# Performance work log

Measured on AMD Instinct MI355X. Metric: run time of the kernel, lower is better.

The kernel has to match this reference:

```python
import jax, jax.numpy as jnp
import numpy as np

NUM_BLOCKS = 6
NUM_HEADS = 8
DIM = 49
SCALE = float(np.sqrt(DIM) + 1e-6)  # sqrt(49)+eps as in the torch code


def setup_inputs() -> dict:
    key = jax.random.key(0)
    ks = jax.random.split(key, 16)
    B, P = 64, 512
    s = 0.1  # keep activations well-scaled
    return {
        "embedding": jax.random.normal(ks[0], (B, P, DIM), jnp.float32),
        "target_labels": jax.random.randint(ks[1], (B,), 0, 10),
        "Wq": jax.random.normal(ks[2], (NUM_BLOCKS, NUM_HEADS, DIM, DIM), jnp.float32) * s,
        "bq": jax.random.normal(ks[3], (NUM_BLOCKS, NUM_HEADS, DIM), jnp.float32) * s,
        "Wk": jax.random.normal(ks[4], (NUM_BLOCKS, NUM_HEADS, DIM, DIM), jnp.float32) * s,
        "bk": jax.random.normal(ks[5], (NUM_BLOCKS, NUM_HEADS, DIM), jnp.float32) * s,
        "Wv": jax.random.normal(ks[6], (NUM_BLOCKS, NUM_HEADS, DIM, DIM), jnp.float32) * s,
        "bv": jax.random.normal(ks[7], (NUM_BLOCKS, NUM_HEADS, DIM), jnp.float32) * s,
        "Wh": jax.random.normal(ks[8], (NUM_BLOCKS, NUM_HEADS, DIM, DIM), jnp.float32) * s,
        "bh": jax.random.normal(ks[9], (NUM_BLOCKS, NUM_HEADS, DIM), jnp.float32) * s,
        "Wout": jax.random.normal(ks[10], (NUM_BLOCKS, DIM, NUM_HEADS * DIM), jnp.float32) * s,
        "W1": jax.random.normal(ks[11], (25, DIM), jnp.float32) * s,
        "b1": jax.random.normal(ks[12], (25,), jnp.float32) * s,
        "W2": jax.random.normal(ks[13], (10, 25), jnp.float32) * s,
        "b2": jax.random.normal(ks[14], (10,), jnp.float32) * s,
    }


def reference(embedding, target_labels, Wq, bq, Wk, bk, Wv, bv, Wh, bh, Wout, W1, b1, W2, b2):
    B, P, D = embedding.shape
    x = embedding
    for l in range(NUM_BLOCKS):  # fixed small structural loop over blocks
        # per-head projections, all heads batched: [B,H,P,D]
        Q = jnp.einsum('bpi,hoi->bhpo', x, Wq[l]) + bq[l][:, None, :]
        K = jnp.einsum('bpi,hoi->bhpo', x, Wk[l]) + bk[l][:, None, :]
        V = jnp.einsum('bpi,hoi->bhpo', x, Wv[l]) + bv[l][:, None, :]
        scores = jnp.einsum('bhpo,bhqo->bhpq', Q, K) / SCALE
        scores = jnp.clip(scores, -30.0, 30.0)
        weights = jax.nn.softmax(scores, axis=-1)
        attn_out = jnp.einsum('bhpq,bhqo->bhpo', weights, V)
        head_out = jnp.einsum('bhpo,hdo->bhpd', attn_out, Wh[l]) + bh[l][:, None, :]
        # concat head outputs along feature dim (head order preserved): [B,P,H*D]
        concat = head_out.transpose(0, 2, 1, 3).reshape(B, P, NUM_HEADS * D)
        # out-projection uses weight only (no bias), as in the torch forward
        x = jnp.einsum('bpc,oc->bpo', concat, Wout[l])
    pooled = x.mean(axis=1)  # [B, D]
    h = jax.nn.relu(pooled @ W1.T + b1)
    logits = h @ W2.T + b2  # [B, 10]
    logp = jax.nn.log_softmax(logits, axis=-1)
    loss = -jnp.take_along_axis(logp, target_labels[:, None], axis=1).mean()
    return loss
```

## Files before the change

kernel.cpp:

```cpp
#include <hip/hip_runtime.h>
#include <hip/hip_bf16.h>
#include <math.h>

#define Bn 64
#define Pn 512
#define Hn 8
#define Ln 6

typedef __bf16 bf16x8 __attribute__((ext_vector_type(8)));
typedef float f32x4 __attribute__((ext_vector_type(4)));

#define VMCNT(n) asm volatile("s_waitcnt vmcnt(" #n ")" ::: "memory")
#define LGKM0()  asm volatile("s_waitcnt lgkmcnt(0)" ::: "memory")

static __device__ __forceinline__ unsigned short f2bf(float f) {
    return __builtin_bit_cast(unsigned short, __float2bfloat16(f));
}
static __device__ __forceinline__ float bf2f(unsigned short v) {
    unsigned int u = ((unsigned int)v) << 16;
    return __builtin_bit_cast(float, u);
}
static __device__ __forceinline__ float fexp2(float x) {
    float r;
    asm("v_exp_f32 %0, %1" : "=v"(r) : "v"(x));
    return r;
}
static __device__ __forceinline__ unsigned cvtpk(float a, float b) {
    unsigned r;
    asm("v_cvt_pk_bf16_f32 %0, %1, %2" : "=v"(r) : "v"(a), "v"(b));
    return r;
}

#define C1F (1.4426950408889634f / 7.000001f)
#define C2F 43.2808512f

__global__ __launch_bounds__(256)
void prep_wqkv_kernel(const float* __restrict__ Wq, const float* __restrict__ Wk,
                      const float* __restrict__ Wv, unsigned short* __restrict__ out) {
    int idx = blockIdx.x * 256 + threadIdx.x;
    if (idx >= Ln * 3 * Hn * 4096) return;
    int i = idx & 63, o = (idx >> 6) & 63, h = (idx >> 12) & 7, t = idx >> 15;
    int mat = t % 3, l = t / 3;
    float v = 0.f;
    if (o < 49 && i < 49) {
        const float* src = (mat == 0) ? Wq : (mat == 1) ? Wk : Wv;
        v = src[(((size_t)(l * Hn + h) * 49) + o) * 49 + i];
    }
    out[idx] = f2bf(v);
}

__global__ __launch_bounds__(256)
void prep_weff_kernel(const float* __restrict__ Wh, const float* __restrict__ bh,
                      const float* __restrict__ Wout,
                      unsigned short* __restrict__ Weff, float* __restrict__ beff) {
    const int NW = Ln * Hn * 4096;
    int idx = blockIdx.x * 256 + threadIdx.x;
    if (idx < NW) {
        int o = idx & 63, o2 = (idx >> 6) & 63, h = (idx >> 12) & 7, l = idx >> 15;
        float s = 0.f;
        if (o < 49 && o2 < 49) {
            const float* wh = Wh + ((size_t)(l * Hn + h) * 49) * 49 + o;
            const float* wo = Wout + ((size_t)l * 49 + o2) * 392 + h * 49;
            for (int dd = 0; dd < 49; ++dd) s = fmaf(wh[dd * 49], wo[dd], s);
        }
        Weff[idx] = f2bf(s);
    } else if (idx < NW + Ln * 49) {
        int j = idx - NW;
        int l = j / 49, o2 = j % 49;
        const float* wo = Wout + ((size_t)l * 49 + o2) * 392;
        const float* bhl = bh + (size_t)l * 392;
        float s = 0.f;
        for (int cc = 0; cc < 392; ++cc) s = fmaf(bhl[cc], wo[cc], s);
        beff[j] = s;
    }
}

__global__ __launch_bounds__(256)
void cast_x_kernel(const float* __restrict__ emb, unsigned short* __restrict__ xbf) {
    int idx = blockIdx.x * 256 + threadIdx.x;
    int row = idx >> 6, col = idx & 63;
    float v = (col < 49) ? emb[(size_t)row * 49 + col] : 0.f;
    xbf[idx] = f2bf(v);
}

__global__ __launch_bounds__(256)
void qkv_mfma_kernel(const unsigned short* __restrict__ xbf,
                     const unsigned short* __restrict__ Wqkv,
                     const float* __restrict__ bq_l, const float* __restrict__ bk_l,
                     const float* __restrict__ bv_l,
                     unsigned short* __restrict__ Qb, unsigned short* __restrict__ Kb,
                     unsigned short* __restrict__ Vt,
                     int b_off, int Bc) {
    __shared__ uint4 xlb4[512];
    __shared__ uint4 wlb4[512];
    __shared__ __align__(16) unsigned short stg[64 * 68];
    __shared__ __align__(16) float blds[1536];
    char* xlb = (char*)xlb4;
    char* wlb = (char*)wlb4;
    const int tid = threadIdx.x;
    const int w = tid >> 6, lane = tid & 63, g = lane >> 4, c = lane & 15;
    const int flat = blockIdx.x;
    const int bl = flat % Bc;
    const int tile = flat / Bc;
    const int r0 = bl * Pn + tile * 64;

    for (int t = tid; t < 1536; t += 256) {
        int mat = t >> 9, rem = t & 511, h = rem >> 6, o = rem & 63;
        const float* bb = (mat == 0) ? bq_l : (mat == 1) ? bk_l : bv_l;
        blds[t] = (o < 49) ? bb[h * 49 + o] : 0.f;
    }
    {
        const unsigned short* xg = xbf + ((size_t)b_off * Pn + r0) * 64;
        #pragma unroll
        for (int i = 0; i < 2; ++i) {
            int chunk = tid + i * 256;
            int row = chunk >> 3, c8 = chunk & 7;
            *(uint4*)(xlb + row * 128 + 16 * (c8 ^ (row & 7))) =
                *(const uint4*)(xg + row * 64 + c8 * 8);
        }
    }
    __syncthreads();

    const int rowa = w * 16 + c;
    bf16x8 a0 = *(const bf16x8*)(xlb + rowa * 128 + 16 * ((g    ) ^ (c & 7)));
    bf16x8 a1 = *(const bf16x8*)(xlb + rowa * 128 + 16 * ((g + 4) ^ (c & 7)));

    for (int panel = 0; panel < 24; ++panel) {
        const int mat = panel >> 3, h = panel & 7;
        const unsigned short* wg = Wqkv + (size_t)panel * 4096;
        #pragma unroll
        for (int i = 0; i < 2; ++i) {
            int chunk = tid + i * 256;
            int row = chunk >> 3, c8 = chunk & 7;
            *(uint4*)(wlb + row * 128 + 16 * (c8 ^ (row & 7))) =
                *(const uint4*)(wg + row * 64 + c8 * 8);
        }
        __syncthreads();

        f32x4 acc[4];
        #pragma unroll
        for (int bt = 0; bt < 4; ++bt) acc[bt] = (f32x4){0.f, 0.f, 0.f, 0.f};
        const float* bbB = blds + mat * 512 + h * 64;

        if (mat < 2) {
            #pragma unroll
            for (int bt = 0; bt < 4; ++bt) {
                int rowb = bt * 16 + c;
                bf16x8 w0 = *(const bf16x8*)(wlb + rowb * 128 + 16 * ((g    ) ^ (rowb & 7)));
                bf16x8 w1 = *(const bf16x8*)(wlb + rowb * 128 + 16 * ((g + 4) ^ (rowb & 7)));
                acc[bt] = __builtin_amdgcn_mfma_f32_16x16x32_bf16(w0, a0, acc[bt], 0, 0, 0);
                acc[bt] = __builtin_amdgcn_mfma_f32_16x16x32_bf16(w1, a1, acc[bt], 0, 0, 0);
            }
            const int p = w * 16 + c;
            #pragma unroll
            for (int bt = 0; bt < 4; ++bt) {
                f32x4 bb4 = *(const f32x4*)(bbB + bt * 16 + 4 * g);
                float v0 = acc[bt][0] + bb4[0];
                float v1 = acc[bt][1] + bb4[1];
                float v2 = acc[bt][2] + bb4[2];
                float v3 = acc[bt][3] + bb4[3];
                if (mat == 0) { v0 *= C1F; v1 *= C1F; v2 *= C1F; v3 *= C1F; }
                if (bt == 3) {
                    float q49 = (mat == 0) ? -C2F : 1.0f;
                    bool g0 = (g == 0);
                    v0 = g0 ? v0 : 0.f;
                    v1 = g0 ? q49 : 0.f;
                    v2 = 0.f; v3 = 0.f;
                }
                uint2 pk = {cvtpk(v0, v1), cvtpk(v2, v3)};
                *(uint2*)((char*)stg + p * 136 + (bt * 16 + 4 * g) * 2) = pk;
            }
        } else {
            #pragma unroll
            for (int bt = 0; bt < 4; ++bt) {
                int rowb = bt * 16 + c;
                bf16x8 w0 = *(const bf16x8*)(wlb + rowb * 128 + 16 * ((g    ) ^ (rowb & 7)));
                bf16x8 w1 = *(const bf16x8*)(wlb + rowb * 128 + 16 * ((g + 4) ^ (rowb & 7)));
                acc[bt] = __builtin_amdgcn_mfma_f32_16x16x32_bf16(a0, w0, acc[bt], 0, 0, 0);
                acc[bt] = __builtin_amdgcn_mfma_f32_16x16x32_bf16(a1, w1, acc[bt], 0, 0, 0);
            }
            #pragma unroll
            for (int bt = 0; bt < 4; ++bt) {
                int d = bt * 16 + c;
                float bbd = bbB[d];
                float v0 = acc[bt][0] + bbd;
                float v1 = acc[bt][1] + bbd;
                float v2 = acc[bt][2] + bbd;
                float v3 = acc[bt][3] + bbd;
                if (bt == 3) {
                    bool is49 = (c == 1);
                    v0 = is49 ? 1.0f : v0;
                    v1 = is49 ? 1.0f : v1;
                    v2 = is49 ? 1.0f : v2;
                    v3 = is49 ? 1.0f : v3;
                }
                uint2 pk = {cvtpk(v0, v1), cvtpk(v2, v3)};
                *(uint2*)((char*)stg + d * 136 + (w * 16 + 4 * g) * 2) = pk;
            }
        }
        __syncthreads();

        if (mat < 2) {
            unsigned short* outp = (mat == 0) ? Qb : Kb;
            #pragma unroll
            for (int i = 0; i < 4; ++i) {
                int chunk = tid + i * 256;
                int prow = chunk >> 4, c4 = chunk & 15;
                uint2 v = *(const uint2*)((const char*)stg + prow * 136 + c4 * 8);
                int rr = r0 + prow;
                int bl2 = rr >> 9, p = rr & 511;
                *(uint2*)(outp + (((size_t)bl2 * Hn + h) * Pn + p) * 64 + c4 * 4) = v;
            }
        } else {
            const int bl2 = r0 >> 9, p0 = r0 & 511;
            #pragma unroll
            for (int i = 0; i < 4; ++i) {
                int chunk = tid + i * 256;
                int drow = chunk >> 4, c4 = chunk & 15;
                uint2 v = *(const uint2*)((const char*)stg + drow * 136 + c4 * 8);
                *(uint2*)(Vt + (((size_t)bl2 * Hn + h) * 64 + drow) * Pn + p0 + c4 * 4) = v;
            }
        }
        __syncthreads();
    }
}

__global__ __launch_bounds__(256, 4)
void attn_head_kernel(const unsigned short* __restrict__ Qb,
                      const unsigned short* __restrict__ Kb,
                      const unsigned short* __restrict__ Vt,
                      unsigned short* __restrict__ AO,
                      int Bc) {
    __shared__ uint4 lds4[2048];
    char* ldsb = (char*)lds4;
    const int tid = threadIdx.x;
    const int w = tid >> 6, lane = tid & 63, g = lane >> 4, c = lane & 15;
    const int flat = blockIdx.x;
    const int x = flat & 7;
    const int qt = (flat >> 3) & 3;
    const int a = flat >> 5;
    const size_t bh = (size_t)(a * 8 + x);
    const int q0 = qt * 128;

    bf16x8 qf[2][2];
    #pragma unroll
    for (int qs = 0; qs < 2; ++qs) {
        const unsigned short* qp = Qb + (bh * Pn + q0 + w * 32 + qs * 16 + c) * 64;
        qf[qs][0] = *(const bf16x8*)(qp + g * 8);
        qf[qs][1] = *(const bf16x8*)(qp + g * 8 + 32);
    }
    f32x4 oacc[2][4];
    #pragma unroll
    for (int qs = 0; qs < 2; ++qs)
        #pragma unroll
        for (int dt = 0; dt < 4; ++dt)
            oacc[qs][dt] = (f32x4){0.f, 0.f, 0.f, 0.f};

    const unsigned short* Kg0 = Kb + bh * (size_t)(Pn * 64);
    const unsigned short* Vg0 = Vt + bh * (size_t)(64 * Pn);

    auto stage = [&](int kt, int buf) {
        const unsigned short* Kg = Kg0 + kt * (64 * 64);
        const unsigned short* Vg = Vg0 + kt * 64;
        #pragma unroll
        for (int j = 0; j < 2; ++j) {
            int chunk = w * 128 + j * 64 + lane;
            int row = chunk >> 3, c8 = chunk & 7;
            int swc = (c8 ^ (row & 7)) << 3;
            __builtin_amdgcn_global_load_lds(
                (const __attribute__((address_space(1))) void*)(Kg + row * 64 + swc),
                (__attribute__((address_space(3))) void*)(ldsb + buf * 8192 + w * 2048 + j * 1024),
                16, 0, 0);
            __builtin_amdgcn_global_load_lds(
                (const __attribute__((address_space(1))) void*)(Vg + (size_t)row * Pn + swc),
                (__attribute__((address_space(3))) void*)(ldsb + 16384 + buf * 8192 + w * 2048 + j * 1024),
                16, 0, 0);
        }
    };

    stage(0, 0);

    #pragma unroll 2
    for (int kt = 0; kt < 8; ++kt) {
        const int cur = kt & 1;
        VMCNT(0);
        __builtin_amdgcn_s_barrier();
        __builtin_amdgcn_sched_barrier(0);
        if (kt < 7) stage(kt + 1, cur ^ 1);
        __builtin_amdgcn_sched_barrier(0);

        char* Klb = ldsb + cur * 8192;
        char* Vlb = ldsb + 16384 + cur * 8192;

        unsigned up01[2][4], up23[2][4];
        #pragma unroll
        for (int t = 0; t < 4; ++t) {
            const int krow = t * 16 + c;
            bf16x8 kf0 = *(const bf16x8*)(Klb + krow * 128 + 16 * ((g    ) ^ (krow & 7)));
            bf16x8 kf1 = *(const bf16x8*)(Klb + krow * 128 + 16 * ((g + 4) ^ (krow & 7)));
            #pragma unroll
            for (int qs = 0; qs < 2; ++qs) {
                f32x4 s4 = {0.f, 0.f, 0.f, 0.f};
                __builtin_amdgcn_s_setprio(1);
                s4 = __builtin_amdgcn_mfma_f32_16x16x32_bf16(kf0, qf[qs][0], s4, 0, 0, 0);
                s4 = __builtin_amdgcn_mfma_f32_16x16x32_bf16(kf1, qf[qs][1], s4, 0, 0, 0);
                __builtin_amdgcn_s_setprio(0);
                float p0 = fexp2(s4[0]);
                float p1 = fexp2(s4[1]);
                float p2 = fexp2(s4[2]);
                float p3 = fexp2(s4[3]);
                up01[qs][t] = cvtpk(p0, p1);
                up23[qs][t] = cvtpk(p2, p3);
            }
        }

        #pragma unroll
        for (int kk = 0; kk < 2; ++kk) {
            bf16x8 pa[2];
            #pragma unroll
            for (int qs = 0; qs < 2; ++qs) {
                unsigned d0 = up01[qs][2 * kk], d2 = up01[qs][2 * kk + 1];
                unsigned d1 = up23[qs][2 * kk], d3 = up23[qs][2 * kk + 1];
                asm("v_permlane32_swap_b32 %0, %1" : "+v"(d0), "+v"(d2));
                asm("v_permlane16_swap_b32 %0, %1" : "+v"(d0), "+v"(d2));
                asm("v_permlane32_swap_b32 %0, %1" : "+v"(d1), "+v"(d3));
                asm("v_permlane16_swap_b32 %0, %1" : "+v"(d1), "+v"(d3));
                uint4 uv = {d0, d1, d2, d3};
                pa[qs] = __builtin_bit_cast(bf16x8, uv);
            }
            __builtin_amdgcn_s_setprio(1);
            #pragma unroll
            for (int dt = 0; dt < 4; ++dt) {
                const int vrow = dt * 16 + c;
                bf16x8 vf = *(const bf16x8*)(Vlb + vrow * 128 + 16 * ((g + 4 * kk) ^ (vrow & 7)));
                oacc[0][dt] = __builtin_amdgcn_mfma_f32_16x16x32_bf16(pa[0], vf, oacc[0][dt], 0, 0, 0);
                oacc[1][dt] = __builtin_amdgcn_mfma_f32_16x16x32_bf16(pa[1], vf, oacc[1][dt], 0, 0, 0);
            }
            __builtin_amdgcn_s_setprio(0);
        }
    }
    __builtin_amdgcn_s_barrier();

    float rinv[2][4];
    #pragma unroll
    for (int qs = 0; qs < 2; ++qs)
        #pragma unroll
        for (int r = 0; r < 4; ++r) {
            float s = __shfl(oacc[qs][3][r], (lane & 48) | 1);
            rinv[qs][r] = 1.0f / s;
        }
    char* stgw = ldsb + w * 4096;
    #pragma unroll
    for (int qs = 0; qs < 2; ++qs)
        #pragma unroll
        for (int dt = 0; dt < 4; ++dt)
            #pragma unroll
            for (int r = 0; r < 4; ++r) {
                int prow = qs * 16 + 4 * g + r;
                int col = dt * 16 + c;
                *(unsigned short*)(stgw + prow * 128 + ((2 * col) ^ ((prow & 7) << 4))) =
                    f2bf(oacc[qs][dt][r] * rinv[qs][r]);
            }
    LGKM0();
    __builtin_amdgcn_sched_barrier(0);
    #pragma unroll
    for (int i = 0; i < 4; ++i) {
        int chunk = i * 64 + lane;
        int row = chunk >> 3, c8 = chunk & 7;
        uint4 v = *(const uint4*)(stgw + row * 128 + 16 * (c8 ^ (row & 7)));
        size_t grow = bh * Pn + q0 + w * 32 + row;
        *(uint4*)(AO + grow * 64 + c8 * 8) = v;
    }
}

__global__ __launch_bounds__(256)
void outqkv_kernel(const unsigned short* __restrict__ AO,
                   const unsigned short* __restrict__ Weffl,
                   const float* __restrict__ beffl,
                   const unsigned short* __restrict__ Wqkv,
                   const float* __restrict__ bq_l, const float* __restrict__ bk_l,
                   const float* __restrict__ bv_l,
                   unsigned short* __restrict__ Qb, unsigned short* __restrict__ Kb,
                   unsigned short* __restrict__ Vt,
                   unsigned short* __restrict__ xout,
                   int last, int b_off, int Bc) {
    __shared__ uint4 lds4[3616];
    __shared__ __align__(16) float blds[1536];
    __shared__ __align__(16) float bldc[64];
    char* ldsb = (char*)lds4;
    unsigned short* stg = (unsigned short*)(ldsb + 49152);
    const int tid = threadIdx.x;
    const int w = tid >> 6, lane = tid & 63, g = lane >> 4, c = lane & 15;
    const int flat = blockIdx.x;
    const int bl = flat % Bc;
    const int tile = flat / Bc;
    const int p0 = tile * 64;
    const int r0 = bl * Pn + p0;

    if (!last) {
        for (int t = tid; t < 1536; t += 256) {
            int mat = t >> 9, rem = t & 511, h = rem >> 6, o = rem & 63;
            const float* bb = (mat == 0) ? bq_l : (mat == 1) ? bk_l : bv_l;
            blds[t] = (o < 49) ? bb[h * 49 + o] : 0.f;
        }
    }
    if (tid < 64) bldc[tid] = (tid < 49) ? beffl[tid] : 0.f;

    const int chunk0 = w * 128 + lane;
    const int rowL0 = chunk0 >> 3, c8L0 = chunk0 & 7;
    const int swc0 = (c8L0 ^ (rowL0 & 7)) << 3;
    const int chunk1 = chunk0 + 64;
    const int rowL1 = chunk1 >> 3, c8L1 = chunk1 & 7;
    const int swc1 = (c8L1 ^ (rowL1 & 7)) << 3;

    auto stageW = [&](const unsigned short* Wg, int buf) {
        __builtin_amdgcn_global_load_lds(
            (const __attribute__((address_space(1))) void*)(Wg + rowL0 * 64 + swc0),
            (__attribute__((address_space(3))) void*)(ldsb + 24576 + buf * 8192 + w * 2048),
            16, 0, 0);
        __builtin_amdgcn_global_load_lds(
            (const __attribute__((address_space(1))) void*)(Wg + rowL1 * 64 + swc1),
            (__attribute__((address_space(3))) void*)(ldsb + 24576 + buf * 8192 + w * 2048 + 1024),
            16, 0, 0);
    };
    auto stageA = [&](const unsigned short* Ag, int buf) {
        __builtin_amdgcn_global_load_lds(
            (const __attribute__((address_space(1))) void*)(Ag + rowL0 * 64 + swc0),
            (__attribute__((address_space(3))) void*)(ldsb + buf * 8192 + w * 2048),
            16, 0, 0);
        __builtin_amdgcn_global_load_lds(
            (const __attribute__((address_space(1))) void*)(Ag + rowL1 * 64 + swc1),
            (__attribute__((address_space(3))) void*)(ldsb + buf * 8192 + w * 2048 + 1024),
            16, 0, 0);
    };

    f32x4 acc[4];
    #pragma unroll
    for (int bt = 0; bt < 4; ++bt) acc[bt] = (f32x4){0.f, 0.f, 0.f, 0.f};

    stageA(AO + (((size_t)bl * Hn + 0) * Pn + p0) * 64, 0);
    stageW(Weffl, 0);
    stageA(AO + (((size_t)bl * Hn + 1) * Pn + p0) * 64, 1);
    stageW(Weffl + 4096, 1);
    for (int h = 0; h < Hn; ++h) {
        const int cur = h % 3;
        if (h < 7) { VMCNT(4); } else { VMCNT(0); }
        __builtin_amdgcn_s_barrier();
        __builtin_amdgcn_sched_barrier(0);
        if (h < 6) {
            stageA(AO + (((size_t)bl * Hn + h + 2) * Pn + p0) * 64, (h + 2) % 3);
            stageW(Weffl + (size_t)(h + 2) * 4096, (h + 2) % 3);
        }
        __builtin_amdgcn_sched_barrier(0);
        char* Alb = ldsb + cur * 8192;
        char* Wlb = ldsb + 24576 + cur * 8192;
        const int rowa = w * 16 + c;
        bf16x8 a0 = *(const bf16x8*)(Alb + rowa * 128 + 16 * ((g    ) ^ (c & 7)));
        bf16x8 a1 = *(const bf16x8*)(Alb + rowa * 128 + 16 * ((g + 4) ^ (c & 7)));
        #pragma unroll
        for (int bt = 0; bt < 4; ++bt) {
            int rowb = bt * 16 + c;
            bf16x8 w0 = *(const bf16x8*)(Wlb + rowb * 128 + 16 * ((g    ) ^ (rowb & 7)));
            bf16x8 w1 = *(const bf16x8*)(Wlb + rowb * 128 + 16 * ((g + 4) ^ (rowb & 7)));
            acc[bt] = __builtin_amdgcn_mfma_f32_16x16x32_bf16(w0, a0, acc[bt], 0, 0, 0);
            acc[bt] = __builtin_amdgcn_mfma_f32_16x16x32_bf16(w1, a1, acc[bt], 0, 0, 0);
        }
    }

    const int p = w * 16 + c;
    if (last) {
        __syncthreads();
        #pragma unroll
        for (int bt = 0; bt < 4; ++bt) {
            f32x4 bb4 = *(const f32x4*)(bldc + bt * 16 + 4 * g);
            uint2 pk = {cvtpk(acc[bt][0] + bb4[0], acc[bt][1] + bb4[1]),
                        cvtpk(acc[bt][2] + bb4[2], acc[bt][3] + bb4[3])};
            *(uint2*)((char*)stg + p * 136 + (bt * 16 + 4 * g) * 2) = pk;
        }
        LGKM0();
        __syncthreads();
        #pragma unroll
        for (int i = 0; i < 4; ++i) {
            int chunk = tid + i * 256;
            int prow = chunk >> 4, c4 = chunk & 15;
            uint2 v = *(const uint2*)((const char*)stg + prow * 136 + c4 * 8);
            size_t grow = (size_t)(b_off + bl) * Pn + p0 + prow;
            *(uint2*)(xout + grow * 64 + c4 * 4) = v;
        }
        return;
    }

    #pragma unroll
    for (int bt = 0; bt < 4; ++bt) {
        f32x4 bb4 = *(const f32x4*)(bldc + bt * 16 + 4 * g);
        uint2 pk = {cvtpk(acc[bt][0] + bb4[0], acc[bt][1] + bb4[1]),
                    cvtpk(acc[bt][2] + bb4[2], acc[bt][3] + bb4[3])};
        *(uint2*)(ldsb + p * 128 + ((2 * (bt * 16 + 4 * g)) ^ ((p & 7) << 4))) = pk;
    }
    stageW(Wqkv, 0);
    LGKM0();
    __builtin_amdgcn_s_barrier();
    __builtin_amdgcn_sched_barrier(0);
    stageW(Wqkv + 4096, 1);

    const int rowa = w * 16 + c;
    bf16x8 a0 = *(const bf16x8*)(ldsb + rowa * 128 + 16 * ((g    ) ^ (c & 7)));
    bf16x8 a1 = *(const bf16x8*)(ldsb + rowa * 128 + 16 * ((g + 4) ^ (c & 7)));

    for (int panel = 0; panel < 24; ++panel) {
        const int mat = panel >> 3, h = panel & 7;
        const int cur = panel % 3;
        if (panel < 23) { VMCNT(2); } else { VMCNT(0); }
        __builtin_amdgcn_s_barrier();
        __builtin_amdgcn_sched_barrier(0);
        if (panel < 22) stageW(Wqkv + (size_t)(panel + 2) * 4096, (panel + 2) % 3);
        __builtin_amdgcn_sched_barrier(0);
        char* Wlb = ldsb + 24576 + cur * 8192;

        f32x4 pacc[4];
        #pragma unroll
        for (int bt = 0; bt < 4; ++bt) pacc[bt] = (f32x4){0.f, 0.f, 0.f, 0.f};
        const float* bbB = blds + mat * 512 + h * 64;

        if (mat < 2) {
            #pragma unroll
            for (int bt = 0; bt < 4; ++bt) {
                int rowb = bt * 16 + c;
                bf16x8 w0 = *(const bf16x8*)(Wlb + rowb * 128 + 16 * ((g    ) ^ (rowb & 7)));
                bf16x8 w1 = *(const bf16x8*)(Wlb + rowb * 128 + 16 * ((g + 4) ^ (rowb & 7)));
                pacc[bt] = __builtin_amdgcn_mfma_f32_16x16x32_bf16(w0, a0, pacc[bt], 0, 0, 0);
                pacc[bt] = __builtin_amdgcn_mfma_f32_16x16x32_bf16(w1, a1, pacc[bt], 0, 0, 0);
            }
            #pragma unroll
            for (int bt = 0; bt < 4; ++bt) {
                f32x4 bb4 = *(const f32x4*)(bbB + bt * 16 + 4 * g);
                float v0 = pacc[bt][0] + bb4[0];
                float v1 = pacc[bt][1] + bb4[1];
                float v2 = pacc[bt][2] + bb4[2];
                float v3 = pacc[bt][3] + bb4[3];
                if (mat == 0) { v0 *= C1F; v1 *= C1F; v2 *= C1F; v3 *= C1F; }
                if (bt == 3) {
                    float q49 = (mat == 0) ? -C2F : 1.0f;
                    bool g0 = (g == 0);
                    v0 = g0 ? v0 : 0.f;
                    v1 = g0 ? q49 : 0.f;
                    v2 = 0.f; v3 = 0.f;
                }
                uint2 pk = {cvtpk(v0, v1), cvtpk(v2, v3)};
                *(uint2*)((char*)stg + p * 136 + (bt * 16 + 4 * g) * 2) = pk;
            }
        } else {
            #pragma unroll
            for (int bt = 0; bt < 4; ++bt) {
                int rowb = bt * 16 + c;
                bf16x8 w0 = *(const bf16x8*)(Wlb + rowb * 128 + 16 * ((g    ) ^ (rowb & 7)));
                bf16x8 w1 = *(const bf16x8*)(Wlb + rowb * 128 + 16 * ((g + 4) ^ (rowb & 7)));
                pacc[bt] = __builtin_amdgcn_mfma_f32_16x16x32_bf16(a0, w0, pacc[bt], 0, 0, 0);
                pacc[bt] = __builtin_amdgcn_mfma_f32_16x16x32_bf16(a1, w1, pacc[bt], 0, 0, 0);
            }
            #pragma unroll
            for (int bt = 0; bt < 4; ++bt) {
                int d = bt * 16 + c;
                float bbd = bbB[d];
                float v0 = pacc[bt][0] + bbd;
                float v1 = pacc[bt][1] + bbd;
                float v2 = pacc[bt][2] + bbd;
                float v3 = pacc[bt][3] + bbd;
                if (bt == 3) {
                    bool is49 = (c == 1);
                    v0 = is49 ? 1.0f : v0;
                    v1 = is49 ? 1.0f : v1;
                    v2 = is49 ? 1.0f : v2;
                    v3 = is49 ? 1.0f : v3;
                }
                uint2 pk = {cvtpk(v0, v1), cvtpk(v2, v3)};
                *(uint2*)((char*)stg + d * 136 + (w * 16 + 4 * g) * 2) = pk;
            }
        }
        LGKM0();
        __builtin_amdgcn_s_barrier();

        if (mat < 2) {
            unsigned short* outp = (mat == 0) ? Qb : Kb;
            #pragma unroll
            for (int i = 0; i < 4; ++i) {
                int chunk = tid + i * 256;
                int prow = chunk >> 4, c4 = chunk & 15;
                uint2 v = *(const uint2*)((const char*)stg + prow * 136 + c4 * 8);
                int rr = r0 + prow;
                int bl2 = rr >> 9, pp = rr & 511;
                *(uint2*)(outp + (((size_t)bl2 * Hn + h) * Pn + pp) * 64 + c4 * 4) = v;
            }
        } else {
            #pragma unroll
            for (int i = 0; i < 4; ++i) {
                int chunk = tid + i * 256;
                int drow = chunk >> 4, c4 = chunk & 15;
                uint2 v = *(const uint2*)((const char*)stg + drow * 136 + c4 * 8);
                *(uint2*)(Vt + (((size_t)bl * Hn + h) * 64 + drow) * Pn + p0 + c4 * 4) = v;
            }
        }
    }
}

__global__ __launch_bounds__(256)
void pool_kernel(const unsigned short* __restrict__ x, float* __restrict__ pooled) {
    __shared__ float red[256];
    const int b = blockIdx.x;
    const int tid = threadIdx.x;
    const int ps = tid >> 6, d = tid & 63;
    float s = 0.f;
    for (int p = ps; p < Pn; p += 4) s += bf2f(x[((size_t)b * Pn + p) * 64 + d]);
    red[tid] = s;
    __syncthreads();
    if (tid < 64) {
        float t = red[tid] + red[tid + 64] + red[tid + 128] + red[tid + 192];
        if (tid < 49) pooled[b * 49 + tid] = t * (1.0f / Pn);
    }
}

__global__ __launch_bounds__(64)
void head_kernel(const float* __restrict__ pooled, const int* __restrict__ labels,
                 const float* __restrict__ W1, const float* __restrict__ b1,
                 const float* __restrict__ W2, const float* __restrict__ b2,
                 float* __restrict__ out) {
    __shared__ float lloss[64];
    const int b = threadIdx.x;
    float pr[49];
    #pragma unroll
    for (int i = 0; i < 49; ++i) pr[i] = pooled[b * 49 + i];
    float hh[25];
    for (int j = 0; j < 25; ++j) {
        float s = b1[j];
        for (int i = 0; i < 49; ++i) s = fmaf(pr[i], W1[j * 49 + i], s);
        hh[j] = fmaxf(s, 0.f);
    }
    float lg[10];
    float m = -1e30f;
    for (int k = 0; k < 10; ++k) {
        float s = b2[k];
        for (int j = 0; j < 25; ++j) s = fmaf(hh[j], W2[k * 25 + j], s);
        lg[k] = s;
        m = fmaxf(m, s);
    }
    float se = 0.f;
    for (int k = 0; k < 10; ++k) se += __expf(lg[k] - m);
    float lse = m + __logf(se);
    int lbl = labels[b];
    lloss[b] = lse - lg[lbl];
    __syncthreads();
    if (b == 0) {
        float s = 0.f;
        for (int i = 0; i < 64; ++i) s += lloss[i];
        out[0] = s * (1.0f / 64.0f);
    }
}

extern "C" void kernel_launch(void* const* d_in, const int* in_sizes, int n_in,
                              void* d_out, int out_size, void* d_ws, size_t ws_size,
                              hipStream_t stream) {
    const float* emb    = (const float*)d_in[0];
    const int*   labels = (const int*)d_in[1];
    const float* Wq = (const float*)d_in[2];
    const float* bq = (const float*)d_in[3];
    const float* Wk = (const float*)d_in[4];
    const float* bk = (const float*)d_in[5];
    const float* Wv = (const float*)d_in[6];
    const float* bv = (const float*)d_in[7];
    const float* Wh = (const float*)d_in[8];
    const float* bhp = (const float*)d_in[9];
    const float* Wout = (const float*)d_in[10];
    const float* W1 = (const float*)d_in[11];
    const float* b1 = (const float*)d_in[12];
    const float* W2 = (const float*)d_in[13];
    const float* b2 = (const float*)d_in[14];
    float* out = (float*)d_out;

    char* base = (char*)d_ws;
    size_t off = 0;
    auto alloc = [&](size_t bytes) {
        off = (off + 255) & ~(size_t)255;
        char* p = base + off;
        off += bytes;
        return p;
    };

    unsigned short* WqkvB = (unsigned short*)alloc((size_t)Ln * 3 * Hn * 4096 * 2);
    unsigned short* WeffB = (unsigned short*)alloc((size_t)Ln * Hn * 4096 * 2);
    float*          beffB = (float*)alloc((size_t)Ln * 49 * 4);
    unsigned short* xA    = (unsigned short*)alloc((size_t)Bn * Pn * 64 * 2);
    unsigned short* xB    = (unsigned short*)alloc((size_t)Bn * Pn * 64 * 2);
    float*          pooled = (float*)alloc((size_t)Bn * 49 * 4);

    const size_t per_b = 4 * ((size_t)Hn * Pn * 64 * 2);
    size_t fixed = (off + 255) & ~(size_t)255;
    int Bc = Bn;
    while (Bc > 8 && fixed + (size_t)Bc * per_b + 4096 > ws_size) Bc >>= 1;

    unsigned short* Qb  = (unsigned short*)alloc((size_t)Bc * Hn * Pn * 64 * 2);
    unsigned short* Kb  = (unsigned short*)alloc((size_t)Bc * Hn * Pn * 64 * 2);
    unsigned short* Vtb = (unsigned short*)alloc((size_t)Bc * Hn * Pn * 64 * 2);
    unsigned short* AOb = (unsigned short*)alloc((size_t)Bc * Hn * Pn * 64 * 2);

    prep_wqkv_kernel<<<(Ln * 3 * Hn * 4096 + 255) / 256, 256, 0, stream>>>(Wq, Wk, Wv, WqkvB);
    prep_weff_kernel<<<(Ln * Hn * 4096 + Ln * 49 + 255) / 256, 256, 0, stream>>>(Wh, bhp, Wout, WeffB, beffB);
    cast_x_kernel<<<(Bn * Pn * 64) / 256, 256, 0, stream>>>(emb, xA);

    for (int b0 = 0; b0 < Bn; b0 += Bc) {
        qkv_mfma_kernel<<<Bc * 8, 256, 0, stream>>>(
            xA, WqkvB, bq, bk, bv, Qb, Kb, Vtb, b0, Bc);
        for (int l = 0; l < Ln; ++l) {
            attn_head_kernel<<<Bc * 32, 256, 0, stream>>>(Qb, Kb, Vtb, AOb, Bc);
            int last = (l == Ln - 1) ? 1 : 0;
            int ln = last ? 0 : (l + 1);
            outqkv_kernel<<<Bc * 8, 256, 0, stream>>>(
                AOb,
                WeffB + (size_t)l * Hn * 4096,
                beffB + (size_t)l * 49,
                WqkvB + (size_t)ln * 3 * Hn * 4096,
                bq + (size_t)ln * Hn * 49,
                bk + (size_t)ln * Hn * 49,
                bv + (size_t)ln * Hn * 49,
                Qb, Kb, Vtb, xB, last, b0, Bc);
        }
    }

    pool_kernel<<<Bn, 256, 0, stream>>>(xB, pooled);
    head_kernel<<<1, 64, 0, stream>>>(pooled, labels, W1, b1, W2, b2, out);
}
```

Measured before the change: 504.5 us.

## Use single-wave blocks in qkv and out-projection kernels, loading weights directly

The qkv and outqkv kernels move from 256-thread blocks covering 64 rows to 64-thread single-wave blocks covering 16 rows, with four times as many blocks. Weight and activation operands are now read straight from global memory into registers, replacing LDS staging and the global_load_lds triple-buffer pipeline, and block-wide barriers become wave-local lgkmcnt waits. This removes barrier and LDS overhead and raises block count and occupancy. The cost is that each wave re-reads the full weight panels from cache, with no staging or prefetch to hide load latency.

```diff
diff --git a/kernel.cpp b/kernel.cpp
--- a/kernel.cpp
+++ b/kernel.cpp
@@ -83,7 +83,7 @@
     xbf[idx] = f2bf(v);
 }
 
-__global__ __launch_bounds__(256)
+__global__ __launch_bounds__(64)
 void qkv_mfma_kernel(const unsigned short* __restrict__ xbf,
                      const unsigned short* __restrict__ Wqkv,
                      const float* __restrict__ bq_l, const float* __restrict__ bk_l,
@@ -91,74 +91,53 @@
                      unsigned short* __restrict__ Qb, unsigned short* __restrict__ Kb,
                      unsigned short* __restrict__ Vt,
                      int b_off, int Bc) {
-    __shared__ uint4 xlb4[512];
-    __shared__ uint4 wlb4[512];
-    __shared__ __align__(16) unsigned short stg[64 * 68];
+    __shared__ __align__(16) unsigned short stg[16 * 68];
+    __shared__ __align__(16) unsigned short stgv[64 * 16];
     __shared__ __align__(16) float blds[1536];
-    char* xlb = (char*)xlb4;
-    char* wlb = (char*)wlb4;
     const int tid = threadIdx.x;
-    const int w = tid >> 6, lane = tid & 63, g = lane >> 4, c = lane & 15;
+    const int g = tid >> 4, c = tid & 15;
     const int flat = blockIdx.x;
     const int bl = flat % Bc;
     const int tile = flat / Bc;
-    const int r0 = bl * Pn + tile * 64;
-
-    for (int t = tid; t < 1536; t += 256) {
+    const int r0 = bl * Pn + tile * 16;
+
+    for (int t = tid; t < 1536; t += 64) {
         int mat = t >> 9, rem = t & 511, h = rem >> 6, o = rem & 63;
         const float* bb = (mat == 0) ? bq_l : (mat == 1) ? bk_l : bv_l;
         blds[t] = (o < 49) ? bb[h * 49 + o] : 0.f;
     }
-    {
-        const unsigned short* xg = xbf + ((size_t)b_off * Pn + r0) * 64;
-        #pragma unroll
-        for (int i = 0; i < 2; ++i) {
-            int chunk = tid + i * 256;
-            int row = chunk >> 3, c8 = chunk & 7;
-            *(uint4*)(xlb + row * 128 + 16 * (c8 ^ (row & 7))) =
-                *(const uint4*)(xg + row * 64 + c8 * 8);
-        }
-    }
-    __syncthreads();
-
-    const int rowa = w * 16 + c;
-    bf16x8 a0 = *(const bf16x8*)(xlb + rowa * 128 + 16 * ((g    ) ^ (c & 7)));
-    bf16x8 a1 = *(const bf16x8*)(xlb + rowa * 128 + 16 * ((g + 4) ^ (c & 7)));
+    LGKM0();
+    __builtin_amdgcn_sched_barrier(0);
+
+    const unsigned short* xg = xbf + ((size_t)b_off * Pn + r0 + c) * 64;
+    bf16x8 a0 = *(const bf16x8*)(xg + g * 8);
+    bf16x8 a1 = *(const bf16x8*)(xg + g * 8 + 32);
 
     for (int panel = 0; panel < 24; ++panel) {
         const int mat = panel >> 3, h = panel & 7;
         const unsigned short* wg = Wqkv + (size_t)panel * 4096;
-        #pragma unroll
-        for (int i = 0; i < 2; ++i) {
-            int chunk = tid + i * 256;
-            int row = chunk >> 3, c8 = chunk & 7;
-            *(uint4*)(wlb + row * 128 + 16 * (c8 ^ (row & 7))) =
-                *(const uint4*)(wg + row * 64 + c8 * 8);
-        }
-        __syncthreads();
-
-        f32x4 acc[4];
-        #pragma unroll
-        for (int bt = 0; bt < 4; ++bt) acc[bt] = (f32x4){0.f, 0.f, 0.f, 0.f};
         const float* bbB = blds + mat * 512 + h * 64;
 
+        f32x4 pacc[4];
+        #pragma unroll
+        for (int bt = 0; bt < 4; ++bt) pacc[bt] = (f32x4){0.f, 0.f, 0.f, 0.f};
+
         if (mat < 2) {
             #pragma unroll
             for (int bt = 0; bt < 4; ++bt) {
-                int rowb = bt * 16 + c;
-                bf16x8 w0 = *(const bf16x8*)(wlb + rowb * 128 + 16 * ((g    ) ^ (rowb & 7)));
-                bf16x8 w1 = *(const bf16x8*)(wlb + rowb * 128 + 16 * ((g + 4) ^ (rowb & 7)));
-                acc[bt] = __builtin_amdgcn_mfma_f32_16x16x32_bf16(w0, a0, acc[bt], 0, 0, 0);
-                acc[bt] = __builtin_amdgcn_mfma_f32_16x16x32_bf16(w1, a1, acc[bt], 0, 0, 0);
-            }
-            const int p = w * 16 + c;
+                const unsigned short* wr = wg + (bt * 16 + c) * 64;
+                bf16x8 w0 = *(const bf16x8*)(wr + g * 8);
+                bf16x8 w1 = *(const bf16x8*)(wr + g * 8 + 32);
+                pacc[bt] = __builtin_amdgcn_mfma_f32_16x16x32_bf16(w0, a0, pacc[bt], 0, 0, 0);
+                pacc[bt] = __builtin_amdgcn_mfma_f32_16x16x32_bf16(w1, a1, pacc[bt], 0, 0, 0);
+            }
             #pragma unroll
             for (int bt = 0; bt < 4; ++bt) {
                 f32x4 bb4 = *(const f32x4*)(bbB + bt * 16 + 4 * g);
-                float v0 = acc[bt][0] + bb4[0];
-                float v1 = acc[bt][1] + bb4[1];
-                float v2 = acc[bt][2] + bb4[2];
-                float v3 = acc[bt][3] + bb4[3];
+                float v0 = pacc[bt][0] + bb4[0];
+                float v1 = pacc[bt][1] + bb4[1];
+                float v2 = pacc[bt][2] + bb4[2];
+                float v3 = pacc[bt][3] + bb4[3];
                 if (mat == 0) { v0 *= C1F; v1 *= C1F; v2 *= C1F; v3 *= C1F; }
                 if (bt == 3) {
                     float q49 = (mat == 0) ? -C2F : 1.0f;
@@ -168,25 +147,37 @@
                     v2 = 0.f; v3 = 0.f;
                 }
                 uint2 pk = {cvtpk(v0, v1), cvtpk(v2, v3)};
-                *(uint2*)((char*)stg + p * 136 + (bt * 16 + 4 * g) * 2) = pk;
+                *(uint2*)((char*)stg + c * 136 + (bt * 16 + 4 * g) * 2) = pk;
+            }
+            LGKM0();
+            __builtin_amdgcn_sched_barrier(0);
+            unsigned short* outp = (mat == 0) ? Qb : Kb;
+            #pragma unroll
+            for (int i = 0; i < 4; ++i) {
+                int chunk = i * 64 + tid;
+                int prow = chunk >> 4, c4 = chunk & 15;
+                uint2 v = *(const uint2*)((const char*)stg + prow * 136 + c4 * 8);
+                int rr = r0 + prow;
+                int bl2 = rr >> 9, pp = rr & 511;
+                *(uint2*)(outp + (((size_t)bl2 * Hn + h) * Pn + pp) * 64 + c4 * 4) = v;
             }
         } else {
             #pragma unroll
             for (int bt = 0; bt < 4; ++bt) {
-                int rowb = bt * 16 + c;
-                bf16x8 w0 = *(const bf16x8*)(wlb + rowb * 128 + 16 * ((g    ) ^ (rowb & 7)));
-                bf16x8 w1 = *(const bf16x8*)(wlb + rowb * 128 + 16 * ((g + 4) ^ (rowb & 7)));
-                acc[bt] = __builtin_amdgcn_mfma_f32_16x16x32_bf16(a0, w0, acc[bt], 0, 0, 0);
-                acc[bt] = __builtin_amdgcn_mfma_f32_16x16x32_bf16(a1, w1, acc[bt], 0, 0, 0);
+                const unsigned short* wr = wg + (bt * 16 + c) * 64;
+                bf16x8 w0 = *(const bf16x8*)(wr + g * 8);
+                bf16x8 w1 = *(const bf16x8*)(wr + g * 8 + 32);
+                pacc[bt] = __builtin_amdgcn_mfma_f32_16x16x32_bf16(a0, w0, pacc[bt], 0, 0, 0);
+                pacc[bt] = __builtin_amdgcn_mfma_f32_16x16x32_bf16(a1, w1, pacc[bt], 0, 0, 0);
             }
             #pragma unroll
             for (int bt = 0; bt < 4; ++bt) {
                 int d = bt * 16 + c;
                 float bbd = bbB[d];
-                float v0 = acc[bt][0] + bbd;
-                float v1 = acc[bt][1] + bbd;
-                float v2 = acc[bt][2] + bbd;
-                float v3 = acc[bt][3] + bbd;
+                float v0 = pacc[bt][0] + bbd;
+                float v1 = pacc[bt][1] + bbd;
+                float v2 = pacc[bt][2] + bbd;
+                float v3 = pacc[bt][3] + bbd;
                 if (bt == 3) {
                     bool is49 = (c == 1);
                     v0 = is49 ? 1.0f : v0;
@@ -195,33 +186,19 @@
                     v3 = is49 ? 1.0f : v3;
                 }
                 uint2 pk = {cvtpk(v0, v1), cvtpk(v2, v3)};
-                *(uint2*)((char*)stg + d * 136 + (w * 16 + 4 * g) * 2) = pk;
-            }
-        }
-        __syncthreads();
-
-        if (mat < 2) {
-            unsigned short* outp = (mat == 0) ? Qb : Kb;
+                *(uint2*)((char*)stgv + d * 32 + g * 8) = pk;
+            }
+            LGKM0();
+            __builtin_amdgcn_sched_barrier(0);
+            const int bl2 = r0 >> 9, p0 = r0 & 511;
             #pragma unroll
             for (int i = 0; i < 4; ++i) {
-                int chunk = tid + i * 256;
-                int prow = chunk >> 4, c4 = chunk & 15;
-                uint2 v = *(const uint2*)((const char*)stg + prow * 136 + c4 * 8);
-                int rr = r0 + prow;
-                int bl2 = rr >> 9, p = rr & 511;
-                *(uint2*)(outp + (((size_t)bl2 * Hn + h) * Pn + p) * 64 + c4 * 4) = v;
-            }
-        } else {
-            const int bl2 = r0 >> 9, p0 = r0 & 511;
-            #pragma unroll
-            for (int i = 0; i < 4; ++i) {
-                int chunk = tid + i * 256;
-                int drow = chunk >> 4, c4 = chunk & 15;
-                uint2 v = *(const uint2*)((const char*)stg + drow * 136 + c4 * 8);
+                int chunk = i * 64 + tid;
+                int drow = chunk >> 2, c4 = chunk & 3;
+                uint2 v = *(const uint2*)((const char*)stgv + drow * 32 + c4 * 8);
                 *(uint2*)(Vt + (((size_t)bl2 * Hn + h) * 64 + drow) * Pn + p0 + c4 * 4) = v;
             }
         }
-        __syncthreads();
     }
 }
 
@@ -373,7 +350,7 @@
     }
 }
 
-__global__ __launch_bounds__(256)
+__global__ __launch_bounds__(64)
 void outqkv_kernel(const unsigned short* __restrict__ AO,
                    const unsigned short* __restrict__ Weffl,
                    const float* __restrict__ beffl,
@@ -384,104 +361,63 @@
                    unsigned short* __restrict__ Vt,
                    unsigned short* __restrict__ xout,
                    int last, int b_off, int Bc) {
-    __shared__ uint4 lds4[3616];
+    __shared__ __align__(16) unsigned short stg[16 * 68];
+    __shared__ __align__(16) unsigned short stgv[64 * 16];
+    __shared__ __align__(16) char xlds[2048];
     __shared__ __align__(16) float blds[1536];
     __shared__ __align__(16) float bldc[64];
-    char* ldsb = (char*)lds4;
-    unsigned short* stg = (unsigned short*)(ldsb + 49152);
     const int tid = threadIdx.x;
-    const int w = tid >> 6, lane = tid & 63, g = lane >> 4, c = lane & 15;
+    const int g = tid >> 4, c = tid & 15;
     const int flat = blockIdx.x;
     const int bl = flat % Bc;
     const int tile = flat / Bc;
-    const int p0 = tile * 64;
+    const int p0 = tile * 16;
     const int r0 = bl * Pn + p0;
 
     if (!last) {
-        for (int t = tid; t < 1536; t += 256) {
+        for (int t = tid; t < 1536; t += 64) {
             int mat = t >> 9, rem = t & 511, h = rem >> 6, o = rem & 63;
             const float* bb = (mat == 0) ? bq_l : (mat == 1) ? bk_l : bv_l;
             blds[t] = (o < 49) ? bb[h * 49 + o] : 0.f;
         }
     }
-    if (tid < 64) bldc[tid] = (tid < 49) ? beffl[tid] : 0.f;
-
-    const int chunk0 = w * 128 + lane;
-    const int rowL0 = chunk0 >> 3, c8L0 = chunk0 & 7;
-    const int swc0 = (c8L0 ^ (rowL0 & 7)) << 3;
-    const int chunk1 = chunk0 + 64;
-    const int rowL1 = chunk1 >> 3, c8L1 = chunk1 & 7;
-    const int swc1 = (c8L1 ^ (rowL1 & 7)) << 3;
-
-    auto stageW = [&](const unsigned short* Wg, int buf) {
-        __builtin_amdgcn_global_load_lds(
-            (const __attribute__((address_space(1))) void*)(Wg + rowL0 * 64 + swc0),
-            (__attribute__((address_space(3))) void*)(ldsb + 24576 + buf * 8192 + w * 2048),
-            16, 0, 0);
-        __builtin_amdgcn_global_load_lds(
-            (const __attribute__((address_space(1))) void*)(Wg + rowL1 * 64 + swc1),
-            (__attribute__((address_space(3))) void*)(ldsb + 24576 + buf * 8192 + w * 2048 + 1024),
-            16, 0, 0);
-    };
-    auto stageA = [&](const unsigned short* Ag, int buf) {
-        __builtin_amdgcn_global_load_lds(
-            (const __attribute__((address_space(1))) void*)(Ag + rowL0 * 64 + swc0),
-            (__attribute__((address_space(3))) void*)(ldsb + buf * 8192 + w * 2048),
-            16, 0, 0);
-        __builtin_amdgcn_global_load_lds(
-            (const __attribute__((address_space(1))) void*)(Ag + rowL1 * 64 + swc1),
-            (__attribute__((address_space(3))) void*)(ldsb + buf * 8192 + w * 2048 + 1024),
-            16, 0, 0);
-    };
+    bldc[tid] = (tid < 49) ? beffl[tid] : 0.f;
+    LGKM0();
+    __builtin_amdgcn_sched_barrier(0);
 
     f32x4 acc[4];
     #pragma unroll
     for (int bt = 0; bt < 4; ++bt) acc[bt] = (f32x4){0.f, 0.f, 0.f, 0.f};
 
-    stageA(AO + (((size_t)bl * Hn + 0) * Pn + p0) * 64, 0);
-    stageW(Weffl, 0);
-    stageA(AO + (((size_t)bl * Hn + 1) * Pn + p0) * 64, 1);
-    stageW(Weffl + 4096, 1);
+    #pragma unroll 2
     for (int h = 0; h < Hn; ++h) {
-        const int cur = h % 3;
-        if (h < 7) { VMCNT(4); } else { VMCNT(0); }
-        __builtin_amdgcn_s_barrier();
-        __builtin_amdgcn_sched_barrier(0);
-        if (h < 6) {
-            stageA(AO + (((size_t)bl * Hn + h + 2) * Pn + p0) * 64, (h + 2) % 3);
-            stageW(Weffl + (size_t)(h + 2) * 4096, (h + 2) % 3);
-        }
-        __builtin_amdgcn_sched_barrier(0);
-        char* Alb = ldsb + cur * 8192;
-        char* Wlb = ldsb + 24576 + cur * 8192;
-        const int rowa = w * 16 + c;
-        bf16x8 a0 = *(const bf16x8*)(Alb + rowa * 128 + 16 * ((g    ) ^ (c & 7)));
-        bf16x8 a1 = *(const bf16x8*)(Alb + rowa * 128 + 16 * ((g + 4) ^ (c & 7)));
+        const unsigned short* Ag = AO + (((size_t)bl * Hn + h) * Pn + p0 + c) * 64;
+        bf16x8 a0 = *(const bf16x8*)(Ag + g * 8);
+        bf16x8 a1 = *(const bf16x8*)(Ag + g * 8 + 32);
+        const unsigned short* Wg = Weffl + (size_t)h * 4096;
         #pragma unroll
         for (int bt = 0; bt < 4; ++bt) {
-            int rowb = bt * 16 + c;
-            bf16x8 w0 = *(const bf16x8*)(Wlb + rowb * 128 + 16 * ((g    ) ^ (rowb & 7)));
-            bf16x8 w1 = *(const bf16x8*)(Wlb + rowb * 128 + 16 * ((g + 4) ^ (rowb & 7)));
+            const unsigned short* wr = Wg + (bt * 16 + c) * 64;
+            bf16x8 w0 = *(const bf16x8*)(wr + g * 8);
+            bf16x8 w1 = *(const bf16x8*)(wr + g * 8 + 32);
             acc[bt] = __builtin_amdgcn_mfma_f32_16x16x32_bf16(w0, a0, acc[bt], 0, 0, 0);
             acc[bt] = __builtin_amdgcn_mfma_f32_16x16x32_bf16(w1, a1, acc[bt], 0, 0, 0);
         }
     }
 
-    const int p = w * 16 + c;
     if (last) {
-        __syncthreads();
         #pragma unroll
         for (int bt = 0; bt < 4; ++bt) {
             f32x4 bb4 = *(const f32x4*)(bldc + bt * 16 + 4 * g);
             uint2 pk = {cvtpk(acc[bt][0] + bb4[0], acc[bt][1] + bb4[1]),
                         cvtpk(acc[bt][2] + bb4[2], acc[bt][3] + bb4[3])};
-            *(uint2*)((char*)stg + p * 136 + (bt * 16 + 4 * g) * 2) = pk;
+            *(uint2*)((char*)stg + c * 136 + (bt * 16 + 4 * g) * 2) = pk;
         }
         LGKM0();
-        __syncthreads();
+        __builtin_amdgcn_sched_barrier(0);
         #pragma unroll
         for (int i = 0; i < 4; ++i) {
-            int chunk = tid + i * 256;
+            int chunk = i * 64 + tid;
             int prow = chunk >> 4, c4 = chunk & 15;
             uint2 v = *(const uint2*)((const char*)stg + prow * 136 + c4 * 8);
             size_t grow = (size_t)(b_off + bl) * Pn + p0 + prow;
@@ -495,39 +431,28 @@
         f32x4 bb4 = *(const f32x4*)(bldc + bt * 16 + 4 * g);
         uint2 pk = {cvtpk(acc[bt][0] + bb4[0], acc[bt][1] + bb4[1]),
                     cvtpk(acc[bt][2] + bb4[2], acc[bt][3] + bb4[3])};
-        *(uint2*)(ldsb + p * 128 + ((2 * (bt * 16 + 4 * g)) ^ ((p & 7) << 4))) = pk;
-    }
-    stageW(Wqkv, 0);
+        *(uint2*)(xlds + c * 128 + ((2 * (bt * 16 + 4 * g)) ^ ((c & 7) << 4))) = pk;
+    }
     LGKM0();
-    __builtin_amdgcn_s_barrier();
     __builtin_amdgcn_sched_barrier(0);
-    stageW(Wqkv + 4096, 1);
-
-    const int rowa = w * 16 + c;
-    bf16x8 a0 = *(const bf16x8*)(ldsb + rowa * 128 + 16 * ((g    ) ^ (c & 7)));
-    bf16x8 a1 = *(const bf16x8*)(ldsb + rowa * 128 + 16 * ((g + 4) ^ (c & 7)));
+    bf16x8 a0 = *(const bf16x8*)(xlds + c * 128 + 16 * ((g    ) ^ (c & 7)));
+    bf16x8 a1 = *(const bf16x8*)(xlds + c * 128 + 16 * ((g + 4) ^ (c & 7)));
 
     for (int panel = 0; panel < 24; ++panel) {
         const int mat = panel >> 3, h = panel & 7;
-        const int cur = panel % 3;
-        if (panel < 23) { VMCNT(2); } else { VMCNT(0); }
-        __builtin_amdgcn_s_barrier();
-        __builtin_amdgcn_sched_barrier(0);
-        if (panel < 22) stageW(Wqkv + (size_t)(panel + 2) * 4096, (panel + 2) % 3);
-        __builtin_amdgcn_sched_barrier(0);
-        char* Wlb = ldsb + 24576 + cur * 8192;
+        const unsigned short* wg = Wqkv + (size_t)panel * 4096;
+        const float* bbB = blds + mat * 512 + h * 64;
 
         f32x4 pacc[4];
         #pragma unroll
         for (int bt = 0; bt < 4; ++bt) pacc[bt] = (f32x4){0.f, 0.f, 0.f, 0.f};
-        const float* bbB = blds + mat * 512 + h * 64;
 
         if (mat < 2) {
             #pragma unroll
             for (int bt = 0; bt < 4; ++bt) {
-                int rowb = bt * 16 + c;
-                bf16x8 w0 = *(const bf16x8*)(Wlb + rowb * 128 + 16 * ((g    ) ^ (rowb & 7)));
-                bf16x8 w1 = *(const bf16x8*)(Wlb + rowb * 128 + 16 * ((g + 4) ^ (rowb & 7)));
+                const unsigned short* wr = wg + (bt * 16 + c) * 64;
+                bf16x8 w0 = *(const bf16x8*)(wr + g * 8);
+                bf16x8 w1 = *(const bf16x8*)(wr + g * 8 + 32);
                 pacc[bt] = __builtin_amdgcn_mfma_f32_16x16x32_bf16(w0, a0, pacc[bt], 0, 0, 0);
                 pacc[bt] = __builtin_amdgcn_mfma_f32_16x16x32_bf16(w1, a1, pacc[bt], 0, 0, 0);
             }
@@ -547,14 +472,26 @@
                     v2 = 0.f; v3 = 0.f;
                 }
                 uint2 pk = {cvtpk(v0, v1), cvtpk(v2, v3)};
-                *(uint2*)((char*)stg + p * 136 + (bt * 16 + 4 * g) * 2) = pk;
+                *(uint2*)((char*)stg + c * 136 + (bt * 16 + 4 * g) * 2) = pk;
+            }
+            LGKM0();
+            __builtin_amdgcn_sched_barrier(0);
+            unsigned short* outp = (mat == 0) ? Qb : Kb;
+            #pragma unroll
+            for (int i = 0; i < 4; ++i) {
+                int chunk = i * 64 + tid;
+                int prow = chunk >> 4, c4 = chunk & 15;
+                uint2 v = *(const uint2*)((const char*)stg + prow * 136 + c4 * 8);
+                int rr = r0 + prow;
+                int bl2 = rr >> 9, pp = rr & 511;
+                *(uint2*)(outp + (((size_t)bl2 * Hn + h) * Pn + pp) * 64 + c4 * 4) = v;
             }
         } else {
             #pragma unroll
             for (int bt = 0; bt < 4; ++bt) {
-                int rowb = bt * 16 + c;
-                bf16x8 w0 = *(const bf16x8*)(Wlb + rowb * 128 + 16 * ((g    ) ^ (rowb & 7)));
-                bf16x8 w1 = *(const bf16x8*)(Wlb + rowb * 128 + 16 * ((g + 4) ^ (rowb & 7)));
+                const unsigned short* wr = wg + (bt * 16 + c) * 64;
+                bf16x8 w0 = *(const bf16x8*)(wr + g * 8);
+                bf16x8 w1 = *(const bf16x8*)(wr + g * 8 + 32);
                 pacc[bt] = __builtin_amdgcn_mfma_f32_16x16x32_bf16(a0, w0, pacc[bt], 0, 0, 0);
                 pacc[bt] = __builtin_amdgcn_mfma_f32_16x16x32_bf16(a1, w1, pacc[bt], 0, 0, 0);
             }
@@ -574,29 +511,15 @@
                     v3 = is49 ? 1.0f : v3;
                 }
                 uint2 pk = {cvtpk(v0, v1), cvtpk(v2, v3)};
-                *(uint2*)((char*)stg + d * 136 + (w * 16 + 4 * g) * 2) = pk;
-            }
-        }
-        LGKM0();
-        __builtin_amdgcn_s_barrier();
-
-        if (mat < 2) {
-            unsigned short* outp = (mat == 0) ? Qb : Kb;
+                *(uint2*)((char*)stgv + d * 32 + g * 8) = pk;
+            }
+            LGKM0();
+            __builtin_amdgcn_sched_barrier(0);
             #pragma unroll
             for (int i = 0; i < 4; ++i) {
-                int chunk = tid + i * 256;
-                int prow = chunk >> 4, c4 = chunk & 15;
-                uint2 v = *(const uint2*)((const char*)stg + prow * 136 + c4 * 8);
-                int rr = r0 + prow;
-                int bl2 = rr >> 9, pp = rr & 511;
-                *(uint2*)(outp + (((size_t)bl2 * Hn + h) * Pn + pp) * 64 + c4 * 4) = v;
-            }
-        } else {
-            #pragma unroll
-            for (int i = 0; i < 4; ++i) {
-                int chunk = tid + i * 256;
-                int drow = chunk >> 4, c4 = chunk & 15;
-                uint2 v = *(const uint2*)((const char*)stg + drow * 136 + c4 * 8);
+                int chunk = i * 64 + tid;
+                int drow = chunk >> 2, c4 = chunk & 3;
+                uint2 v = *(const uint2*)((const char*)stgv + drow * 32 + c4 * 8);
                 *(uint2*)(Vt + (((size_t)bl * Hn + h) * 64 + drow) * Pn + p0 + c4 * 4) = v;
             }
         }
@@ -707,13 +630,13 @@
     cast_x_kernel<<<(Bn * Pn * 64) / 256, 256, 0, stream>>>(emb, xA);
 
     for (int b0 = 0; b0 < Bn; b0 += Bc) {
-        qkv_mfma_kernel<<<Bc * 8, 256, 0, stream>>>(
+        qkv_mfma_kernel<<<Bc * 32, 64, 0, stream>>>(
             xA, WqkvB, bq, bk, bv, Qb, Kb, Vtb, b0, Bc);
         for (int l = 0; l < Ln; ++l) {
             attn_head_kernel<<<Bc * 32, 256, 0, stream>>>(Qb, Kb, Vtb, AOb, Bc);
             int last = (l == Ln - 1) ? 1 : 0;
             int ln = last ? 0 : (l + 1);
-            outqkv_kernel<<<Bc * 8, 256, 0, stream>>>(
+            outqkv_kernel<<<Bc * 32, 64, 0, stream>>>(
                 AOb,
                 WeffB + (size_t)l * Hn * 4096,
                 beffB + (size_t)l * 49,
```

Result: slower. 761.1 us (+50.8%).
